# Kernel optimization log

Measured on AMD Instinct MI355X. Metric: run time of the kernel, lower is better.

The kernel has to match this reference:

```python
import jax, jax.numpy as jnp
import numpy as np

DIM_MODEL = 1024
NHEAD = 16
DIM_HEAD = DIM_MODEL // NHEAD


def setup_inputs() -> dict:
    key = jax.random.key(0)
    k1, k2, k3, k4 = jax.random.split(key, 4)
    x = jax.random.normal(k1, (4, 2048, DIM_MODEL), dtype=jnp.float32)
    # nn.Linear weights: PyTorch stores [out, in]; we keep [in, out] for x @ W.
    s = 1.0 / np.sqrt(DIM_MODEL)
    w_qkv = jax.random.uniform(k2, (DIM_MODEL, 3 * DIM_MODEL), jnp.float32, -s, s)
    w_out = jax.random.uniform(k3, (DIM_MODEL, DIM_MODEL), jnp.float32, -s, s)
    b_out = jax.random.uniform(k4, (DIM_MODEL,), jnp.float32, -s, s)
    return {"x": x, "w_qkv": w_qkv, "w_out": w_out, "b_out": b_out}


def reference(x, w_qkv, w_out, b_out):
    b, n, _ = x.shape
    scale = DIM_HEAD ** -0.5
    qkv = x @ w_qkv                              # [b, n, 3*dim]
    q, k, v = jnp.split(qkv, 3, axis=-1)
    def split_heads(t):                          # [b, n, h*d] -> [b, h, n, d]
        return t.reshape(b, n, NHEAD, DIM_HEAD).transpose(0, 2, 1, 3)
    q, k, v = split_heads(q), split_heads(k), split_heads(v)
    attn = jnp.einsum('bhnd,bhmd->bhnm', q, k) * scale
    attn = jax.nn.softmax(attn, axis=-1)
    out = jnp.einsum('bhnm,bhmd->bhnd', attn, v)
    out = out.transpose(0, 2, 1, 3).reshape(b, n, NHEAD * DIM_HEAD)
    return out @ w_out + b_out
```

## Files before the change

### kernel.cpp

```cpp
#include <hip/hip_runtime.h>
#include <math.h>

#define DM   1024
#define NH   16
#define SEQ  2048
#define BATCH 4
#define QSCALE 0.18033688011112042f

typedef __attribute__((ext_vector_type(8)))  short short8;
typedef __attribute__((ext_vector_type(4)))  float f32x4;
typedef __attribute__((ext_vector_type(16))) float f32x16;

static __device__ __forceinline__ unsigned short f2bf(float f) {
    unsigned u = __float_as_uint(f);
    unsigned r = (u + 0x7fffu + ((u >> 16) & 1u)) >> 16;
    return (unsigned short)r;
}

#define GLD(gp, lp) __builtin_amdgcn_global_load_lds( \
    (const __attribute__((address_space(1))) void*)(gp), \
    (__attribute__((address_space(3))) void*)(lp), 16, 0, 0)

__global__ __launch_bounds__(256) void prep_all(
    const float* __restrict__ x, unsigned short* __restrict__ x_h,
    const float* __restrict__ w_qkv, unsigned short* __restrict__ wqT_h,
    const float* __restrict__ w_out, unsigned short* __restrict__ woT_h)
{
    __shared__ float t[32][33];
    const int bid = blockIdx.x;
    const int tid = threadIdx.x;
    if (bid < 8192) {
        int i = bid * 256 + tid;
        float4 v = reinterpret_cast<const float4*>(x)[i];
        ushort4 h;
        h.x = f2bf(v.x); h.y = f2bf(v.y); h.z = f2bf(v.z); h.w = f2bf(v.w);
        reinterpret_cast<ushort4*>(x_h)[i] = h;
        return;
    }
    const float* in;
    unsigned short* outT;
    int K = DM, N, n0, k0;
    if (bid < 8192 + 3072) {
        int bb = bid - 8192;
        in = w_qkv; outT = wqT_h; N = 3 * DM;
        n0 = (bb % 96) * 32; k0 = (bb / 96) * 32;
    } else {
        int bb = bid - 8192 - 3072;
        in = w_out; outT = woT_h; N = DM;
        n0 = (bb % 32) * 32; k0 = (bb / 32) * 32;
    }
    const int tx = tid & 31, ty = tid >> 5;
    #pragma unroll
    for (int r = 0; r < 32; r += 8)
        t[ty + r][tx] = in[(size_t)(k0 + ty + r) * N + n0 + tx];
    __syncthreads();
    #pragma unroll
    for (int r = 0; r < 32; r += 8)
        outT[(size_t)(n0 + ty + r) * K + k0 + tx] = f2bf(t[tx][ty + r]);
}

__global__ __launch_bounds__(256) void gemm_qkv(
    const unsigned short* __restrict__ Ah, const unsigned short* __restrict__ Bh,
    unsigned short* __restrict__ Qh, unsigned short* __restrict__ Kph,
    unsigned short* __restrict__ Vph, int M, int N, int K)
{
    __shared__ __align__(16) unsigned short sAh[128 * 32];
    __shared__ __align__(16) unsigned short sBh[128 * 32];

    const int tid = threadIdx.x;
    const int l = tid & 63, w = tid >> 6;
    const int wr = w >> 1, wc = w & 1;

    int nwg = gridDim.x * gridDim.y;
    int lin = blockIdx.x + gridDim.x * blockIdx.y;
    int cpx = nwg >> 3;
    int nl = (lin & 7) * cpx + (lin >> 3);
    const int bm = (nl / gridDim.y) * 128, bn = (nl % gridDim.y) * 128;

    const int srow = w * 32 + (l >> 2);
    const int scol = (((l & 3) ^ ((l >> 3) & 3))) * 8;
    const size_t a0 = (size_t)(bm + srow) * K + scol;
    const size_t a1 = (size_t)(bm + srow + 16) * K + scol;
    const size_t b0 = (size_t)(bn + srow) * K + scol;
    const size_t b1 = (size_t)(bn + srow + 16) * K + scol;

    const int fr = l & 15;
    const int hi = l >> 4;
    const int csw = (hi ^ ((fr >> 1) & 3)) * 8;

    f32x4 acc[4][4];
    #pragma unroll
    for (int i = 0; i < 4; ++i)
        #pragma unroll
        for (int j = 0; j < 4; ++j)
            acc[i][j] = (f32x4){0.f, 0.f, 0.f, 0.f};

    for (int k0 = 0; k0 < K; k0 += 32) {
        __syncthreads();
        GLD(Ah + a0 + k0, sAh + w * 1024);
        GLD(Ah + a1 + k0, sAh + w * 1024 + 512);
        GLD(Bh + b0 + k0, sBh + w * 1024);
        GLD(Bh + b1 + k0, sBh + w * 1024 + 512);
        __syncthreads();

        short8 vah[4], vbh[4];
        #pragma unroll
        for (int i = 0; i < 4; ++i) {
            int ar = (wr * 64 + i * 16 + fr) * 32 + csw;
            int br = (wc * 64 + i * 16 + fr) * 32 + csw;
            vah[i] = *reinterpret_cast<const short8*>(&sAh[ar]);
            vbh[i] = *reinterpret_cast<const short8*>(&sBh[br]);
        }
        __builtin_amdgcn_s_setprio(1);
        #pragma unroll
        for (int i = 0; i < 4; ++i)
            #pragma unroll
            for (int j = 0; j < 4; ++j)
                acc[i][j] = __builtin_amdgcn_mfma_f32_16x16x32_bf16(vah[i], vbh[j], acc[i][j], 0, 0, 0);
        __builtin_amdgcn_s_setprio(0);
    }

    #pragma unroll
    for (int i = 0; i < 4; ++i) {
        #pragma unroll
        for (int j = 0; j < 4; ++j) {
            int row0 = bm + wr * 64 + i * 16 + (l >> 4) * 4;
            int col  = bn + wc * 64 + j * 16 + fr;
            if (col < 1024) {
                #pragma unroll
                for (int r = 0; r < 4; ++r)
                    Qh[(size_t)(row0 + r) * 1024 + col] = f2bf(acc[i][j][r] * QSCALE);
            } else if (col < 2048) {
                int sec = col - 1024, head = sec >> 6, d = sec & 63;
                int pK = ((d >> 4) << 1) | ((d >> 3) & 1);
                int d7 = d & 7;
                #pragma unroll
                for (int r = 0; r < 4; ++r) {
                    int row = row0 + r;
                    int bb = row >> 11, seq = row & 2047;
                    int kt = seq >> 6, k64 = seq & 63;
                    int p = ((k64 >> 5) << 3) + pK;
                    size_t addr = ((((size_t)(bb * 16 + head) * 32 + kt) * 512)
                                   + p * 32 + (k64 & 31)) * 8 + d7;
                    Kph[addr] = f2bf(acc[i][j][r]);
                }
            } else {
                int sec = col - 2048, head = sec >> 6, d = sec & 63;
                int row = row0;
                int bb = row >> 11, seq = row & 2047;
                int kt = seq >> 6, k64 = seq & 63, k16 = k64 & 15;
                int p = ((d >> 5) << 3) + ((k64 >> 4) << 1) + ((k16 >> 2) & 1);
                int jbase = (k16 >> 3) << 2;
                size_t chunk = (((size_t)(bb * 16 + head) * 32 + kt) * 512
                                + p * 32 + (d & 31));
                ushort4 v4;
                #pragma unroll
                for (int r = 0; r < 4; ++r)
                    ((unsigned short*)&v4)[r] = f2bf(acc[i][j][r]);
                *reinterpret_cast<ushort4*>(Vph + chunk * 8 + jbase) = v4;
            }
        }
    }
}

__global__ __launch_bounds__(256) void gemm_out(
    const unsigned short* __restrict__ Ah, const unsigned short* __restrict__ Bh,
    const float* __restrict__ bias, float* __restrict__ C, int M, int N, int K)
{
    __shared__ __align__(16) unsigned short sAh[128 * 32];
    __shared__ __align__(16) unsigned short sBh[128 * 32];

    const int tid = threadIdx.x;
    const int l = tid & 63, w = tid >> 6;
    const int wr = w >> 1, wc = w & 1;

    int nwg = gridDim.x * gridDim.y;
    int lin = blockIdx.x + gridDim.x * blockIdx.y;
    int cpx = nwg >> 3;
    int nl = (lin & 7) * cpx + (lin >> 3);
    const int bm = (nl / gridDim.y) * 128, bn = (nl % gridDim.y) * 128;

    const int srow = w * 32 + (l >> 2);
    const int scol = (((l & 3) ^ ((l >> 3) & 3))) * 8;
    const size_t a0 = (size_t)(bm + srow) * K + scol;
    const size_t a1 = (size_t)(bm + srow + 16) * K + scol;
    const size_t b0 = (size_t)(bn + srow) * K + scol;
    const size_t b1 = (size_t)(bn + srow + 16) * K + scol;

    const int fr = l & 15;
    const int hi = l >> 4;
    const int csw = (hi ^ ((fr >> 1) & 3)) * 8;

    f32x4 acc[4][4];
    #pragma unroll
    for (int i = 0; i < 4; ++i)
        #pragma unroll
        for (int j = 0; j < 4; ++j)
            acc[i][j] = (f32x4){0.f, 0.f, 0.f, 0.f};

    for (int k0 = 0; k0 < K; k0 += 32) {
        __syncthreads();
        GLD(Ah + a0 + k0, sAh + w * 1024);
        GLD(Ah + a1 + k0, sAh + w * 1024 + 512);
        GLD(Bh + b0 + k0, sBh + w * 1024);
        GLD(Bh + b1 + k0, sBh + w * 1024 + 512);
        __syncthreads();

        short8 vah[4], vbh[4];
        #pragma unroll
        for (int i = 0; i < 4; ++i) {
            int ar = (wr * 64 + i * 16 + fr) * 32 + csw;
            int br = (wc * 64 + i * 16 + fr) * 32 + csw;
            vah[i] = *reinterpret_cast<const short8*>(&sAh[ar]);
            vbh[i] = *reinterpret_cast<const short8*>(&sBh[br]);
        }
        __builtin_amdgcn_s_setprio(1);
        #pragma unroll
        for (int i = 0; i < 4; ++i)
            #pragma unroll
            for (int j = 0; j < 4; ++j)
                acc[i][j] = __builtin_amdgcn_mfma_f32_16x16x32_bf16(vah[i], vbh[j], acc[i][j], 0, 0, 0);
        __builtin_amdgcn_s_setprio(0);
    }

    #pragma unroll
    for (int i = 0; i < 4; ++i) {
        #pragma unroll
        for (int j = 0; j < 4; ++j) {
            int row = bm + wr * 64 + i * 16 + (l >> 4) * 4;
            int col = bn + wc * 64 + j * 16 + fr;
            float bb = bias[col];
            #pragma unroll
            for (int r = 0; r < 4; ++r)
                C[(size_t)(row + r) * N + col] = acc[i][j][r] + bb;
        }
    }
}

__global__ __launch_bounds__(256, 3) void flash_attn_mfma(
    const unsigned short* __restrict__ Qh,
    const unsigned short* __restrict__ Kph,
    const unsigned short* __restrict__ Vph,
    unsigned short* __restrict__ out_hi)
{
    __shared__ __align__(16) unsigned short sK[2][4096];
    __shared__ __align__(16) unsigned short sV[2][4096];

    int lin = blockIdx.x + 16 * blockIdx.y + 256 * blockIdx.z;
    int nlid = (lin & 7) * 128 + (lin >> 3);
    const int qt = nlid & 15, head = (nlid >> 4) & 15, b = nlid >> 8;

    const int tid = threadIdx.x;
    const int l = tid & 63, w = tid >> 6;
    const int q5 = l & 31, hf = l >> 5;

    const int bh = b * NH + head;
    const size_t kvb = (size_t)bh * 32 * 512 * 8;

    #define STAGE_KV(cbuf, kt_) do {                                          \
        _Pragma("unroll")                                                     \
        for (int i2 = 0; i2 < 2; ++i2) {                                      \
            int ch = (w * 2 + i2) * 64 + l;                                   \
            size_t s8 = kvb + ((size_t)(kt_) * 512 + ch) * 8;                 \
            GLD(Kph + s8, (char*)&sK[cbuf][0] + ch * 16);                     \
            GLD(Vph + s8, (char*)&sV[cbuf][0] + ch * 16);                     \
        }                                                                     \
    } while (0)

    const int qrow = qt * 128 + w * 32 + q5;
    short8 qhr[4];
    {
        const size_t qb = ((size_t)b * SEQ + qrow) * 1024 + head * 64;
        #pragma unroll
        for (int s = 0; s < 4; ++s)
            qhr[s] = *reinterpret_cast<const short8*>(Qh + qb + s * 16 + hf * 8);
    }

    float l_ = 0.f;
    f32x16 oacc0, oacc1, fz;
    #pragma unroll
    for (int r = 0; r < 16; ++r) { oacc0[r] = 0.f; oacc1[r] = 0.f; fz[r] = 0.f; }

    union FragU { unsigned u[4]; short8 s8; };
    short8 pbh[4];

    STAGE_KV(0, 0);
    int cur = 0;

    for (int kt = 0; kt < SEQ / 64; ++kt) {
        __syncthreads();
        if (kt + 1 < SEQ / 64) STAGE_KV(cur ^ 1, kt + 1);

        const char* kb = (const char*)&sK[cur][0] + l * 16;

        f32x16 sacc0, sacc1;
        __builtin_amdgcn_s_setprio(1);
        {
            short8 k0h = *reinterpret_cast<const short8*>(kb);
            short8 k1h = *reinterpret_cast<const short8*>(kb + 4 * 1024);
            sacc0 = __builtin_amdgcn_mfma_f32_32x32x16_bf16(k0h, qhr[0], fz, 0, 0, 0);
            sacc1 = __builtin_amdgcn_mfma_f32_32x32x16_bf16(k1h, qhr[0], fz, 0, 0, 0);
        }
        #pragma unroll
        for (int s = 1; s < 4; ++s) {
            short8 k0h = *reinterpret_cast<const short8*>(kb + s * 1024);
            short8 k1h = *reinterpret_cast<const short8*>(kb + (4 + s) * 1024);
            sacc0 = __builtin_amdgcn_mfma_f32_32x32x16_bf16(k0h, qhr[s], sacc0, 0, 0, 0);
            sacc1 = __builtin_amdgcn_mfma_f32_32x32x16_bf16(k1h, qhr[s], sacc1, 0, 0, 0);
        }
        __builtin_amdgcn_s_setprio(0);

        float ssum = 0.f;
        #pragma unroll
        for (int jt = 0; jt < 2; ++jt) {
            float pv[16];
            #pragma unroll
            for (int r = 0; r < 16; ++r) {
                float sv = (jt == 0) ? sacc0[r] : sacc1[r];
                pv[r] = __builtin_amdgcn_exp2f(sv);
                ssum += pv[r];
            }
            FragU f0, f1;
            asm("v_cvt_pk_bf16_f32 %0, %1, %2" : "=v"(f0.u[0]) : "v"(pv[0]),  "v"(pv[1]));
            asm("v_cvt_pk_bf16_f32 %0, %1, %2" : "=v"(f0.u[1]) : "v"(pv[2]),  "v"(pv[3]));
            asm("v_cvt_pk_bf16_f32 %0, %1, %2" : "=v"(f0.u[2]) : "v"(pv[4]),  "v"(pv[5]));
            asm("v_cvt_pk_bf16_f32 %0, %1, %2" : "=v"(f0.u[3]) : "v"(pv[6]),  "v"(pv[7]));
            asm("v_cvt_pk_bf16_f32 %0, %1, %2" : "=v"(f1.u[0]) : "v"(pv[8]),  "v"(pv[9]));
            asm("v_cvt_pk_bf16_f32 %0, %1, %2" : "=v"(f1.u[1]) : "v"(pv[10]), "v"(pv[11]));
            asm("v_cvt_pk_bf16_f32 %0, %1, %2" : "=v"(f1.u[2]) : "v"(pv[12]), "v"(pv[13]));
            asm("v_cvt_pk_bf16_f32 %0, %1, %2" : "=v"(f1.u[3]) : "v"(pv[14]), "v"(pv[15]));
            pbh[jt * 2 + 0] = f0.s8;
            pbh[jt * 2 + 1] = f1.s8;
        }
        l_ += ssum;

        const char* vb = (const char*)&sV[cur][0] + l * 16;
        __builtin_amdgcn_s_setprio(1);
        #pragma unroll
        for (int kpv = 0; kpv < 4; ++kpv) {
            short8 v0h = *reinterpret_cast<const short8*>(vb + kpv * 1024);
            short8 v1h = *reinterpret_cast<const short8*>(vb + (4 + kpv) * 1024);
            oacc0 = __builtin_amdgcn_mfma_f32_32x32x16_bf16(v0h, pbh[kpv], oacc0, 0, 0, 0);
            oacc1 = __builtin_amdgcn_mfma_f32_32x32x16_bf16(v1h, pbh[kpv], oacc1, 0, 0, 0);
        }
        __builtin_amdgcn_s_setprio(0);
        cur ^= 1;
    }

    l_ += __shfl_xor(l_, 32);
    float linv = 1.f / l_;
    #pragma unroll
    for (int dt = 0; dt < 2; ++dt) {
        #pragma unroll
        for (int rq = 0; rq < 4; ++rq) {
            int dbase = dt * 32 + rq * 8 + 4 * hf;
            ushort4 h4;
            #pragma unroll
            for (int c = 0; c < 4; ++c) {
                float v = ((dt == 0) ? oacc0[rq * 4 + c] : oacc1[rq * 4 + c]) * linv;
                ((unsigned short*)&h4)[c] = f2bf(v);
            }
            size_t o = ((size_t)b * SEQ + qrow) * DM + head * 64 + dbase;
            *reinterpret_cast<ushort4*>(out_hi + o) = h4;
        }
    }
    #undef STAGE_KV
}

extern "C" void kernel_launch(void* const* d_in, const int* in_sizes, int n_in,
                              void* d_out, int out_size, void* d_ws, size_t ws_size,
                              hipStream_t stream) {
    const float* x     = (const float*)d_in[0];
    const float* w_qkv = (const float*)d_in[1];
    const float* w_out = (const float*)d_in[2];
    const float* b_out = (const float*)d_in[3];
    float* out = (float*)d_out;

    const int M = BATCH * SEQ;

    char* ws = (char*)d_ws;
    unsigned short* x_h   = (unsigned short*)ws;                         ws += (size_t)M * DM * 2;
    unsigned short* Qh    = (unsigned short*)ws;                         ws += (size_t)M * DM * 2;
    unsigned short* Kp_h  = (unsigned short*)ws;                         ws += (size_t)M * DM * 2;
    unsigned short* Vp_h  = (unsigned short*)ws;                         ws += (size_t)M * DM * 2;
    unsigned short* wqT_h = (unsigned short*)ws;                         ws += (size_t)3072 * DM * 2;
    unsigned short* woT_h = (unsigned short*)ws;                         ws += (size_t)DM * DM * 2;
    unsigned short* at_hi = (unsigned short*)ws;

    dim3 blk(256);

    prep_all<<<dim3(8192 + 3072 + 1024), blk, 0, stream>>>(
        x, x_h, w_qkv, wqT_h, w_out, woT_h);

    gemm_qkv<<<dim3(M / 128, 3 * DM / 128), blk, 0, stream>>>(
        x_h, wqT_h, Qh, Kp_h, Vp_h, M, 3 * DM, DM);

    flash_attn_mfma<<<dim3(SEQ / 128, NH, BATCH), blk, 0, stream>>>(
        Qh, Kp_h, Vp_h, at_hi);

    gemm_out<<<dim3(M / 128, DM / 128), blk, 0, stream>>>(
        at_hi, woT_h, b_out, out, M, DM, DM);
}
```

Measured before the change: 188.9 us.

## Load K/V fragments directly from global memory instead of LDS double-buffering

The flash-attention kernel drops the shared-memory double buffer for K and V and the per-tile __syncthreads. Each wave now reads its packed K and V MFMA fragments straight from global memory into registers. This removes LDS traffic and block-wide barriers. In exchange, every wave issues its own global loads for the same K/V tile, four times the global/L2 traffic, and load latency is no longer hidden by prefetching the next tile.

```diff
diff --git a/kernel.cpp b/kernel.cpp
--- a/kernel.cpp
+++ b/kernel.cpp
@@ -243,9 +243,6 @@
     const unsigned short* __restrict__ Vph,
     unsigned short* __restrict__ out_hi)
 {
-    __shared__ __align__(16) unsigned short sK[2][4096];
-    __shared__ __align__(16) unsigned short sV[2][4096];
-
     int lin = blockIdx.x + 16 * blockIdx.y + 256 * blockIdx.z;
     int nlid = (lin & 7) * 128 + (lin >> 3);
     const int qt = nlid & 15, head = (nlid >> 4) & 15, b = nlid >> 8;
@@ -255,17 +252,8 @@
     const int q5 = l & 31, hf = l >> 5;
 
     const int bh = b * NH + head;
-    const size_t kvb = (size_t)bh * 32 * 512 * 8;
-
-    #define STAGE_KV(cbuf, kt_) do {                                          \
-        _Pragma("unroll")                                                     \
-        for (int i2 = 0; i2 < 2; ++i2) {                                      \
-            int ch = (w * 2 + i2) * 64 + l;                                   \
-            size_t s8 = kvb + ((size_t)(kt_) * 512 + ch) * 8;                 \
-            GLD(Kph + s8, (char*)&sK[cbuf][0] + ch * 16);                     \
-            GLD(Vph + s8, (char*)&sV[cbuf][0] + ch * 16);                     \
-        }                                                                     \
-    } while (0)
+    const unsigned short* Kb = Kph + (size_t)bh * 32 * 4096 + (size_t)l * 8;
+    const unsigned short* Vb = Vph + (size_t)bh * 32 * 4096 + (size_t)l * 8;
 
     const int qrow = qt * 128 + w * 32 + q5;
     short8 qhr[4];
@@ -284,31 +272,30 @@
     union FragU { unsigned u[4]; short8 s8; };
     short8 pbh[4];
 
-    STAGE_KV(0, 0);
-    int cur = 0;
-
     for (int kt = 0; kt < SEQ / 64; ++kt) {
-        __syncthreads();
-        if (kt + 1 < SEQ / 64) STAGE_KV(cur ^ 1, kt + 1);
-
-        const char* kb = (const char*)&sK[cur][0] + l * 16;
+        const unsigned short* kp = Kb + (size_t)kt * 4096;
+        const unsigned short* vp = Vb + (size_t)kt * 4096;
+
+        short8 kf[8];
+        #pragma unroll
+        for (int s = 0; s < 8; ++s)
+            kf[s] = *reinterpret_cast<const short8*>(kp + s * 512);
 
         f32x16 sacc0, sacc1;
         __builtin_amdgcn_s_setprio(1);
-        {
-            short8 k0h = *reinterpret_cast<const short8*>(kb);
-            short8 k1h = *reinterpret_cast<const short8*>(kb + 4 * 1024);
-            sacc0 = __builtin_amdgcn_mfma_f32_32x32x16_bf16(k0h, qhr[0], fz, 0, 0, 0);
-            sacc1 = __builtin_amdgcn_mfma_f32_32x32x16_bf16(k1h, qhr[0], fz, 0, 0, 0);
-        }
+        sacc0 = __builtin_amdgcn_mfma_f32_32x32x16_bf16(kf[0], qhr[0], fz, 0, 0, 0);
+        sacc1 = __builtin_amdgcn_mfma_f32_32x32x16_bf16(kf[4], qhr[0], fz, 0, 0, 0);
         #pragma unroll
         for (int s = 1; s < 4; ++s) {
-            short8 k0h = *reinterpret_cast<const short8*>(kb + s * 1024);
-            short8 k1h = *reinterpret_cast<const short8*>(kb + (4 + s) * 1024);
-            sacc0 = __builtin_amdgcn_mfma_f32_32x32x16_bf16(k0h, qhr[s], sacc0, 0, 0, 0);
-            sacc1 = __builtin_amdgcn_mfma_f32_32x32x16_bf16(k1h, qhr[s], sacc1, 0, 0, 0);
+            sacc0 = __builtin_amdgcn_mfma_f32_32x32x16_bf16(kf[s],     qhr[s], sacc0, 0, 0, 0);
+            sacc1 = __builtin_amdgcn_mfma_f32_32x32x16_bf16(kf[4 + s], qhr[s], sacc1, 0, 0, 0);
         }
         __builtin_amdgcn_s_setprio(0);
+
+        short8 vf[8];
+        #pragma unroll
+        for (int s = 0; s < 8; ++s)
+            vf[s] = *reinterpret_cast<const short8*>(vp + s * 512);
 
         float ssum = 0.f;
         #pragma unroll
@@ -334,17 +321,13 @@
         }
         l_ += ssum;
 
-        const char* vb = (const char*)&sV[cur][0] + l * 16;
         __builtin_amdgcn_s_setprio(1);
         #pragma unroll
         for (int kpv = 0; kpv < 4; ++kpv) {
-            short8 v0h = *reinterpret_cast<const short8*>(vb + kpv * 1024);
-            short8 v1h = *reinterpret_cast<const short8*>(vb + (4 + kpv) * 1024);
-            oacc0 = __builtin_amdgcn_mfma_f32_32x32x16_bf16(v0h, pbh[kpv], oacc0, 0, 0, 0);
-            oacc1 = __builtin_amdgcn_mfma_f32_32x32x16_bf16(v1h, pbh[kpv], oacc1, 0, 0, 0);
+            oacc0 = __builtin_amdgcn_mfma_f32_32x32x16_bf16(vf[kpv],     pbh[kpv], oacc0, 0, 0, 0);
+            oacc1 = __builtin_amdgcn_mfma_f32_32x32x16_bf16(vf[4 + kpv], pbh[kpv], oacc1, 0, 0, 0);
         }
         __builtin_amdgcn_s_setprio(0);
-        cur ^= 1;
     }
 
     l_ += __shfl_xor(l_, 32);
@@ -364,7 +347,6 @@
             *reinterpret_cast<ushort4*>(out_hi + o) = h4;
         }
     }
-    #undef STAGE_KV
 }
 
 extern "C" void kernel_launch(void* const* d_in, const int* in_sizes, int n_in,
```

New measurement: 200.5 us. +6.1%, slower.

## Process two 32-row query sub-tiles per wave in flash attention

Applied to the files above, without the earlier changes.

Each wave now handles 64 query rows, kept as two 32-row sub-tiles, so the attention block covers 256 queries and the grid along the sequence is halved. Each K/V fragment read from LDS is reused across twice as many MFMAs, which halves LDS traffic and global K/V staging per query. The cost is roughly double the accumulator and Q registers, so the occupancy hint drops from 3 to 2 blocks per CU. With 512 blocks instead of 1024 there are also fewer waves available to hide latency.

```diff
diff --git a/kernel.cpp b/kernel.cpp
--- a/kernel.cpp
+++ b/kernel.cpp
@@ -237,7 +237,7 @@
     }
 }
 
-__global__ __launch_bounds__(256, 3) void flash_attn_mfma(
+__global__ __launch_bounds__(256, 2) void flash_attn_mfma(
     const unsigned short* __restrict__ Qh,
     const unsigned short* __restrict__ Kph,
     const unsigned short* __restrict__ Vph,
@@ -246,9 +246,9 @@
     __shared__ __align__(16) unsigned short sK[2][4096];
     __shared__ __align__(16) unsigned short sV[2][4096];
 
-    int lin = blockIdx.x + 16 * blockIdx.y + 256 * blockIdx.z;
-    int nlid = (lin & 7) * 128 + (lin >> 3);
-    const int qt = nlid & 15, head = (nlid >> 4) & 15, b = nlid >> 8;
+    int lin = blockIdx.x + 8 * blockIdx.y + 128 * blockIdx.z;
+    int nlid = (lin & 7) * 64 + (lin >> 3);
+    const int qt = nlid & 7, head = (nlid >> 3) & 15, b = nlid >> 7;
 
     const int tid = threadIdx.x;
     const int l = tid & 63, w = tid >> 6;
@@ -267,22 +267,27 @@
         }                                                                     \
     } while (0)
 
-    const int qrow = qt * 128 + w * 32 + q5;
-    short8 qhr[4];
-    {
-        const size_t qb = ((size_t)b * SEQ + qrow) * 1024 + head * 64;
+    const int qrow0 = qt * 256 + w * 64 + q5;
+    short8 qhr[2][4];
+    #pragma unroll
+    for (int sub = 0; sub < 2; ++sub) {
+        const size_t qb = ((size_t)b * SEQ + qrow0 + 32 * sub) * 1024 + head * 64;
         #pragma unroll
         for (int s = 0; s < 4; ++s)
-            qhr[s] = *reinterpret_cast<const short8*>(Qh + qb + s * 16 + hf * 8);
-    }
-
-    float l_ = 0.f;
-    f32x16 oacc0, oacc1, fz;
-    #pragma unroll
-    for (int r = 0; r < 16; ++r) { oacc0[r] = 0.f; oacc1[r] = 0.f; fz[r] = 0.f; }
+            qhr[sub][s] = *reinterpret_cast<const short8*>(Qh + qb + s * 16 + hf * 8);
+    }
+
+    float l_[2] = {0.f, 0.f};
+    f32x16 oacc[2][2], fz;
+    #pragma unroll
+    for (int r = 0; r < 16; ++r) {
+        oacc[0][0][r] = 0.f; oacc[0][1][r] = 0.f;
+        oacc[1][0][r] = 0.f; oacc[1][1][r] = 0.f;
+        fz[r] = 0.f;
+    }
 
     union FragU { unsigned u[4]; short8 s8; };
-    short8 pbh[4];
+    short8 pbh[2][4];
 
     STAGE_KV(0, 0);
     int cur = 0;
@@ -293,75 +298,90 @@
 
         const char* kb = (const char*)&sK[cur][0] + l * 16;
 
-        f32x16 sacc0, sacc1;
+        f32x16 sacc[2][2];
         __builtin_amdgcn_s_setprio(1);
         {
-            short8 k0h = *reinterpret_cast<const short8*>(kb);
-            short8 k1h = *reinterpret_cast<const short8*>(kb + 4 * 1024);
-            sacc0 = __builtin_amdgcn_mfma_f32_32x32x16_bf16(k0h, qhr[0], fz, 0, 0, 0);
-            sacc1 = __builtin_amdgcn_mfma_f32_32x32x16_bf16(k1h, qhr[0], fz, 0, 0, 0);
+            short8 k0 = *reinterpret_cast<const short8*>(kb);
+            short8 k1 = *reinterpret_cast<const short8*>(kb + 4 * 1024);
+            #pragma unroll
+            for (int sub = 0; sub < 2; ++sub) {
+                sacc[sub][0] = __builtin_amdgcn_mfma_f32_32x32x16_bf16(k0, qhr[sub][0], fz, 0, 0, 0);
+                sacc[sub][1] = __builtin_amdgcn_mfma_f32_32x32x16_bf16(k1, qhr[sub][0], fz, 0, 0, 0);
+            }
         }
         #pragma unroll
         for (int s = 1; s < 4; ++s) {
-            short8 k0h = *reinterpret_cast<const short8*>(kb + s * 1024);
-            short8 k1h = *reinterpret_cast<const short8*>(kb + (4 + s) * 1024);
-            sacc0 = __builtin_amdgcn_mfma_f32_32x32x16_bf16(k0h, qhr[s], sacc0, 0, 0, 0);
-            sacc1 = __builtin_amdgcn_mfma_f32_32x32x16_bf16(k1h, qhr[s], sacc1, 0, 0, 0);
+            short8 k0 = *reinterpret_cast<const short8*>(kb + s * 1024);
+            short8 k1 = *reinterpret_cast<const short8*>(kb + (4 + s) * 1024);
+            #pragma unroll
+            for (int sub = 0; sub < 2; ++sub) {
+                sacc[sub][0] = __builtin_amdgcn_mfma_f32_32x32x16_bf16(k0, qhr[sub][s], sacc[sub][0], 0, 0, 0);
+                sacc[sub][1] = __builtin_amdgcn_mfma_f32_32x32x16_bf16(k1, qhr[sub][s], sacc[sub][1], 0, 0, 0);
+            }
         }
         __builtin_amdgcn_s_setprio(0);
 
-        float ssum = 0.f;
-        #pragma unroll
-        for (int jt = 0; jt < 2; ++jt) {
-            float pv[16];
-            #pragma unroll
-            for (int r = 0; r < 16; ++r) {
-                float sv = (jt == 0) ? sacc0[r] : sacc1[r];
-                pv[r] = __builtin_amdgcn_exp2f(sv);
-                ssum += pv[r];
-            }
-            FragU f0, f1;
-            asm("v_cvt_pk_bf16_f32 %0, %1, %2" : "=v"(f0.u[0]) : "v"(pv[0]),  "v"(pv[1]));
-            asm("v_cvt_pk_bf16_f32 %0, %1, %2" : "=v"(f0.u[1]) : "v"(pv[2]),  "v"(pv[3]));
-            asm("v_cvt_pk_bf16_f32 %0, %1, %2" : "=v"(f0.u[2]) : "v"(pv[4]),  "v"(pv[5]));
-            asm("v_cvt_pk_bf16_f32 %0, %1, %2" : "=v"(f0.u[3]) : "v"(pv[6]),  "v"(pv[7]));
-            asm("v_cvt_pk_bf16_f32 %0, %1, %2" : "=v"(f1.u[0]) : "v"(pv[8]),  "v"(pv[9]));
-            asm("v_cvt_pk_bf16_f32 %0, %1, %2" : "=v"(f1.u[1]) : "v"(pv[10]), "v"(pv[11]));
-            asm("v_cvt_pk_bf16_f32 %0, %1, %2" : "=v"(f1.u[2]) : "v"(pv[12]), "v"(pv[13]));
-            asm("v_cvt_pk_bf16_f32 %0, %1, %2" : "=v"(f1.u[3]) : "v"(pv[14]), "v"(pv[15]));
-            pbh[jt * 2 + 0] = f0.s8;
-            pbh[jt * 2 + 1] = f1.s8;
-        }
-        l_ += ssum;
+        #pragma unroll
+        for (int sub = 0; sub < 2; ++sub) {
+            float ssum = 0.f;
+            #pragma unroll
+            for (int jt = 0; jt < 2; ++jt) {
+                float pv[16];
+                #pragma unroll
+                for (int r = 0; r < 16; ++r) {
+                    pv[r] = __builtin_amdgcn_exp2f(sacc[sub][jt][r]);
+                    ssum += pv[r];
+                }
+                FragU f0, f1;
+                asm("v_cvt_pk_bf16_f32 %0, %1, %2" : "=v"(f0.u[0]) : "v"(pv[0]),  "v"(pv[1]));
+                asm("v_cvt_pk_bf16_f32 %0, %1, %2" : "=v"(f0.u[1]) : "v"(pv[2]),  "v"(pv[3]));
+                asm("v_cvt_pk_bf16_f32 %0, %1, %2" : "=v"(f0.u[2]) : "v"(pv[4]),  "v"(pv[5]));
+                asm("v_cvt_pk_bf16_f32 %0, %1, %2" : "=v"(f0.u[3]) : "v"(pv[6]),  "v"(pv[7]));
+                asm("v_cvt_pk_bf16_f32 %0, %1, %2" : "=v"(f1.u[0]) : "v"(pv[8]),  "v"(pv[9]));
+                asm("v_cvt_pk_bf16_f32 %0, %1, %2" : "=v"(f1.u[1]) : "v"(pv[10]), "v"(pv[11]));
+                asm("v_cvt_pk_bf16_f32 %0, %1, %2" : "=v"(f1.u[2]) : "v"(pv[12]), "v"(pv[13]));
+                asm("v_cvt_pk_bf16_f32 %0, %1, %2" : "=v"(f1.u[3]) : "v"(pv[14]), "v"(pv[15]));
+                pbh[sub][jt * 2 + 0] = f0.s8;
+                pbh[sub][jt * 2 + 1] = f1.s8;
+            }
+            l_[sub] += ssum;
+        }
 
         const char* vb = (const char*)&sV[cur][0] + l * 16;
         __builtin_amdgcn_s_setprio(1);
         #pragma unroll
         for (int kpv = 0; kpv < 4; ++kpv) {
-            short8 v0h = *reinterpret_cast<const short8*>(vb + kpv * 1024);
-            short8 v1h = *reinterpret_cast<const short8*>(vb + (4 + kpv) * 1024);
-            oacc0 = __builtin_amdgcn_mfma_f32_32x32x16_bf16(v0h, pbh[kpv], oacc0, 0, 0, 0);
-            oacc1 = __builtin_amdgcn_mfma_f32_32x32x16_bf16(v1h, pbh[kpv], oacc1, 0, 0, 0);
+            short8 v0 = *reinterpret_cast<const short8*>(vb + kpv * 1024);
+            short8 v1 = *reinterpret_cast<const short8*>(vb + (4 + kpv) * 1024);
+            #pragma unroll
+            for (int sub = 0; sub < 2; ++sub) {
+                oacc[sub][0] = __builtin_amdgcn_mfma_f32_32x32x16_bf16(v0, pbh[sub][kpv], oacc[sub][0], 0, 0, 0);
+                oacc[sub][1] = __builtin_amdgcn_mfma_f32_32x32x16_bf16(v1, pbh[sub][kpv], oacc[sub][1], 0, 0, 0);
+            }
         }
         __builtin_amdgcn_s_setprio(0);
         cur ^= 1;
     }
 
-    l_ += __shfl_xor(l_, 32);
-    float linv = 1.f / l_;
-    #pragma unroll
-    for (int dt = 0; dt < 2; ++dt) {
-        #pragma unroll
-        for (int rq = 0; rq < 4; ++rq) {
-            int dbase = dt * 32 + rq * 8 + 4 * hf;
-            ushort4 h4;
-            #pragma unroll
-            for (int c = 0; c < 4; ++c) {
-                float v = ((dt == 0) ? oacc0[rq * 4 + c] : oacc1[rq * 4 + c]) * linv;
-                ((unsigned short*)&h4)[c] = f2bf(v);
-            }
-            size_t o = ((size_t)b * SEQ + qrow) * DM + head * 64 + dbase;
-            *reinterpret_cast<ushort4*>(out_hi + o) = h4;
+    #pragma unroll
+    for (int sub = 0; sub < 2; ++sub) {
+        float lt = l_[sub] + __shfl_xor(l_[sub], 32);
+        float linv = 1.f / lt;
+        const int qrow = qrow0 + 32 * sub;
+        #pragma unroll
+        for (int dt = 0; dt < 2; ++dt) {
+            #pragma unroll
+            for (int rq = 0; rq < 4; ++rq) {
+                int dbase = dt * 32 + rq * 8 + 4 * hf;
+                ushort4 h4;
+                #pragma unroll
+                for (int c = 0; c < 4; ++c) {
+                    float v = oacc[sub][dt][rq * 4 + c] * linv;
+                    ((unsigned short*)&h4)[c] = f2bf(v);
+                }
+                size_t o = ((size_t)b * SEQ + qrow) * DM + head * 64 + dbase;
+                *reinterpret_cast<ushort4*>(out_hi + o) = h4;
+            }
         }
     }
     #undef STAGE_KV
@@ -395,7 +415,7 @@
     gemm_qkv<<<dim3(M / 128, 3 * DM / 128), blk, 0, stream>>>(
         x_h, wqT_h, Qh, Kp_h, Vp_h, M, 3 * DM, DM);
 
-    flash_attn_mfma<<<dim3(SEQ / 128, NH, BATCH), blk, 0, stream>>>(
+    flash_attn_mfma<<<dim3(SEQ / 256, NH, BATCH), blk, 0, stream>>>(
         Qh, Kp_h, Vp_h, at_hi);
 
     gemm_out<<<dim3(M / 128, DM / 128), blk, 0, stream>>>(
```

After: 193.4 us. 2.4% more time.
